# Kernel optimization log

Measured on AMD Instinct MI355X. Metric: run time of the kernel, lower is better.

Reference implementation:

```python
import jax, jax.numpy as jnp
from jax import lax
import numpy as np

WIN = 11
SIGMA = 1.5
VAL_RANGE = 10.0
C1 = (0.01 * VAL_RANGE) ** 2
C2 = (0.03 * VAL_RANGE) ** 2


def _gauss_window():
    # matches pytorch-ssim create_window: normalized 1D gaussian, outer product
    g = np.exp(-((np.arange(WIN) - WIN // 2) ** 2) / (2.0 * SIGMA ** 2))
    g = g / g.sum()
    return jnp.asarray(np.outer(g, g), jnp.float32)


def _blur(x, win):
    # depthwise 11x11 gaussian conv, padding=0 (VALID), per pytorch-ssim with padd=0
    k = x.shape[1]
    kern = jnp.broadcast_to(win[None, None], (k, 1, WIN, WIN)).astype(x.dtype)
    return lax.conv_general_dilated(x, kern, (1, 1), 'VALID', feature_group_count=k)


def setup_inputs() -> dict:
    key = jax.random.key(0)
    ks = jax.random.split(key, 7)
    B, C, H, W = 8, 64, 256, 256
    x = jax.random.normal(ks[0], (B, C, H, W), jnp.float32)
    mask = jax.random.randint(ks[1], (B, H, W), 0, 2, jnp.int32)
    conv_w = jax.random.normal(ks[2], (1, 3, 3, 1), jnp.float32) * 0.3
    w1 = jax.random.normal(ks[3], (C, C), jnp.float32) * (1.0 / np.sqrt(C))
    b1 = jax.random.normal(ks[4], (C,), jnp.float32) * 0.01
    w2 = jax.random.normal(ks[5], (C, C), jnp.float32) * (1.0 / np.sqrt(C))
    b2 = jax.random.normal(ks[6], (C,), jnp.float32) * 0.01
    return {'x': x, 'mask': mask, 'conv_w': conv_w, 'w1': w1, 'b1': b1, 'w2': w2, 'b2': b2}


def reference(x, mask, conv_w, w1, b1, w2, b2):
    B, C, H, W = x.shape
    m = mask.astype(x.dtype)[:, None]  # [B,1,H,W]

    # ChannelPool: max/mean/min over channel dim -> [B,3,H,W]
    xc = jnp.stack([x.max(axis=1), x.mean(axis=1), x.min(axis=1)], axis=1)

    # ChannelNorm: masked per-sample, per-channel mean / unbiased std; zero outside mask
    n = m.sum(axis=(2, 3), keepdims=True)                       # [B,1,1,1]
    mean = (xc * m).sum(axis=(2, 3), keepdims=True) / n
    var = (((xc - mean) ** 2) * m).sum(axis=(2, 3), keepdims=True) / (n - 1.0)
    xf = (xc - mean) / jnp.sqrt(var) * m                        # [B,3,H,W]

    # Pairwise SSIM between xf channels (3) and x channels (C), vectorized
    win = _gauss_window()
    mu_f = _blur(xf, win)                                       # [B,3,H',W']
    mu_x = _blur(x, win)                                        # [B,C,H',W']
    ef2 = _blur(xf * xf, win)
    ex2 = _blur(x * x, win)
    prod = (xf[:, :, None] * x[:, None]).reshape(B, 3 * C, H, W)
    Hp, Wp = H - WIN + 1, W - WIN + 1
    exf = _blur(prod, win).reshape(B, 3, C, Hp, Wp)

    mu1 = mu_f[:, :, None]                                      # [B,3,1,H',W']
    mu2 = mu_x[:, None]                                         # [B,1,C,H',W']
    s1 = ef2[:, :, None] - mu1 ** 2
    s2 = ex2[:, None] - mu2 ** 2
    s12 = exf - mu1 * mu2
    ssim_map = ((2 * mu1 * mu2 + C1) * (2 * s12 + C2)) / ((mu1 ** 2 + mu2 ** 2 + C1) * (s1 + s2 + C2))
    ssim_info = ssim_map.mean(axis=(3, 4))                      # [B,3,C]

    # spatial Conv2d(3,1,(3,1),pad=(1,0)) on [B,3,C,1], then ReLU, MLP, Sigmoid
    h = lax.conv_general_dilated(ssim_info[..., None], conv_w, (1, 1), ((1, 1), (0, 0)))
    h = jax.nn.relu(h).reshape(B, C)
    h = jax.nn.relu(h @ w1.T + b1)
    h = jax.nn.sigmoid(h @ w2.T + b2)
    return h, ssim_info
```

## Files before the change

### kernel.cpp

```cpp
#include <hip/hip_runtime.h>
#include <cmath>

#define Bn   8
#define Cn   64
#define HWc  65536
#define HPc  246
#define HPWPc 60516
#define C1v  0.01f
#define C2v  0.09f

static __device__ __forceinline__ void gauss11(float* gw) {
    double gg[11]; double s = 0.0;
#pragma unroll
    for (int j = 0; j < 11; ++j) { double d = (double)(j - 5); gg[j] = exp(-(d * d) / 4.5); s += gg[j]; }
#pragma unroll
    for (int j = 0; j < 11; ++j) gw[j] = (float)(gg[j] / s);
}

static __device__ __forceinline__ float4 f4z() { return make_float4(0.f, 0.f, 0.f, 0.f); }
static __device__ __forceinline__ float4 f4scale(float g, const float4 v) {
    return make_float4(g * v.x, g * v.y, g * v.z, g * v.w);
}
static __device__ __forceinline__ void f4add(float4& a, const float4 v) {
    a.x += v.x; a.y += v.y; a.z += v.z; a.w += v.w;
}
static __device__ __forceinline__ void f4fma(float4& a, const float4 u, const float4 v) {
    a.x = fmaf(u.x, v.x, a.x); a.y = fmaf(u.y, v.y, a.y);
    a.z = fmaf(u.z, v.z, a.z); a.w = fmaf(u.w, v.w, a.w);
}

static __device__ __forceinline__ void hblur4(const float* vb, int base, const float* gw, float* out4) {
    float w[14];
#pragma unroll
    for (int m = 0; m < 14; ++m) w[m] = vb[base + m];
#pragma unroll
    for (int j = 0; j < 4; ++j) {
        float s = 0.f;
#pragma unroll
        for (int k = 0; k < 11; ++k) s = fmaf(gw[k], w[j + k], s);
        out4[j] = s;
    }
}

__global__ __launch_bounds__(256) void k1_stats(const float* __restrict__ x, const int* __restrict__ mask,
                                                float* __restrict__ xcf, float* __restrict__ stats) {
    const int b = blockIdx.y;
    const int p0 = blockIdx.x * 1024 + threadIdx.x * 4;
    const float4* xp = (const float4*)(x + (size_t)b * Cn * HWc) + (p0 >> 2);
    float4 v = xp[0];
    float4 vmax = v, vmin = v, vsum = v;
#pragma unroll 4
    for (int c = 1; c < Cn; ++c) {
        float4 u = xp[(size_t)c * (HWc / 4)];
        vmax.x = fmaxf(vmax.x, u.x); vmax.y = fmaxf(vmax.y, u.y);
        vmax.z = fmaxf(vmax.z, u.z); vmax.w = fmaxf(vmax.w, u.w);
        vmin.x = fminf(vmin.x, u.x); vmin.y = fminf(vmin.y, u.y);
        vmin.z = fminf(vmin.z, u.z); vmin.w = fminf(vmin.w, u.w);
        vsum.x += u.x; vsum.y += u.y; vsum.z += u.z; vsum.w += u.w;
    }
    float4 vmean = make_float4(vsum.x * (1.f / 64.f), vsum.y * (1.f / 64.f),
                               vsum.z * (1.f / 64.f), vsum.w * (1.f / 64.f));
    *(float4*)(xcf + (size_t)(b * 3 + 0) * HWc + p0) = vmax;
    *(float4*)(xcf + (size_t)(b * 3 + 1) * HWc + p0) = vmean;
    *(float4*)(xcf + (size_t)(b * 3 + 2) * HWc + p0) = vmin;
    int4 mv = *(const int4*)(mask + (size_t)b * HWc + p0);
    float m0 = (float)mv.x, m1 = (float)mv.y, m2 = (float)mv.z, m3 = (float)mv.w;
    float r[7];
    r[0] = m0 + m1 + m2 + m3;
    r[1] = vmax.x * m0 + vmax.y * m1 + vmax.z * m2 + vmax.w * m3;
    r[2] = vmean.x * m0 + vmean.y * m1 + vmean.z * m2 + vmean.w * m3;
    r[3] = vmin.x * m0 + vmin.y * m1 + vmin.z * m2 + vmin.w * m3;
    r[4] = vmax.x * vmax.x * m0 + vmax.y * vmax.y * m1 + vmax.z * vmax.z * m2 + vmax.w * vmax.w * m3;
    r[5] = vmean.x * vmean.x * m0 + vmean.y * vmean.y * m1 + vmean.z * vmean.z * m2 + vmean.w * vmean.w * m3;
    r[6] = vmin.x * vmin.x * m0 + vmin.y * vmin.y * m1 + vmin.z * vmin.z * m2 + vmin.w * vmin.w * m3;
#pragma unroll
    for (int k = 0; k < 7; ++k) {
        float vv = r[k];
#pragma unroll
        for (int off = 32; off > 0; off >>= 1) vv += __shfl_down(vv, off);
        if ((threadIdx.x & 63) == 0) atomicAdd(&stats[b * 8 + k], vv);
    }
}

__global__ __launch_bounds__(256) void k3_xf(float* __restrict__ xcf, const int* __restrict__ mask,
                                             const float* __restrict__ stats) {
    const int b = blockIdx.z, i = blockIdx.y;
    const int p0 = blockIdx.x * 1024 + threadIdx.x * 4;
    const float* st = stats + b * 8;
    const float n = st[0];
    const float s1 = st[1 + i], s2 = st[4 + i];
    const float mean = s1 / n;
    const float var = (s2 - s1 * s1 / n) / (n - 1.0f);
    const float rstd = rsqrtf(var);
    float4* p = (float4*)(xcf + (size_t)(b * 3 + i) * HWc + p0);
    float4 v = *p;
    int4 mv = *(const int4*)(mask + (size_t)b * HWc + p0);
    v.x = (v.x - mean) * rstd * (float)mv.x;
    v.y = (v.y - mean) * rstd * (float)mv.y;
    v.z = (v.z - mean) * rstd * (float)mv.z;
    v.w = (v.w - mean) * rstd * (float)mv.w;
    *p = v;
}

__global__ __launch_bounds__(256) void k4_blur3(const float* __restrict__ xf, float* __restrict__ muf,
                                                float* __restrict__ ef2g) {
    __shared__ __align__(16) float fin[42 * 44];
    __shared__ __align__(16) float vba[32 * 52];
    __shared__ __align__(16) float vbb[32 * 52];
    const int t = threadIdx.x;
    const int bi = blockIdx.z;
    const int y0 = blockIdx.y * 32, x0 = blockIdx.x * 32;
    float gw[11]; gauss11(gw);
    const float* src = xf + (size_t)bi * HWc;
    for (int q = t; q < 42 * 11; q += 256) {
        int row = q / 11, cg = q % 11;
        int gr = min(y0 + row, 255), gc = min(x0 + cg * 4, 252);
        *(float4*)&fin[row * 44 + cg * 4] = *(const float4*)(src + gr * 256 + gc);
    }
    __syncthreads();
    if (t < 88) {
        int rg = t / 11, cg = t % 11, colo = cg * 4;
        float4 aa[4], ab[4];
#pragma unroll
        for (int r = 0; r < 4; ++r) { aa[r] = f4z(); ab[r] = f4z(); }
#pragma unroll
        for (int k = 0; k < 14; ++k) {
            float4 v = *(const float4*)&fin[(4 * rg + k) * 44 + colo];
#pragma unroll
            for (int r = 0; r < 4; ++r) {
                int kk = k - r;
                if (kk >= 0 && kk <= 10) {
                    float4 tv = f4scale(gw[kk], v);
                    f4add(aa[r], tv);
                    f4fma(ab[r], tv, v);
                }
            }
        }
#pragma unroll
        for (int r = 0; r < 4; ++r) {
            int so = (4 * rg + r) * 52 + colo;
            *(float4*)&vba[so] = aa[r];
            *(float4*)&vbb[so] = ab[r];
        }
    }
    __syncthreads();
    {
        int erow = t >> 3, ecg = t & 7;
        int oyy = y0 + erow;
        int base = erow * 52 + ecg * 4;
        float o1[4], o2[4];
        hblur4(vba, base, gw, o1);
        hblur4(vbb, base, gw, o2);
        if (oyy < HPc) {
            size_t ob = (size_t)bi * HPWPc + (size_t)oyy * HPc;
#pragma unroll
            for (int j = 0; j < 4; ++j) {
                int ox = x0 + ecg * 4 + j;
                if (ox < HPc) { muf[ob + ox] = o1[j]; ef2g[ob + ox] = o2[j]; }
            }
        }
    }
}

__global__ __launch_bounds__(256, 2) void k5_main(const float* __restrict__ x, const float* __restrict__ xf,
                                                  const float* __restrict__ muf, const float* __restrict__ ef2g,
                                                  float* __restrict__ ssum) {
    __shared__ __align__(16) float xin[42 * 44];
    __shared__ __align__(16) float f0in[42 * 44];
    __shared__ __align__(16) float f1in[42 * 44];
    __shared__ __align__(16) float f2in[42 * 44];
    __shared__ __align__(16) float vbx[32 * 52];
    __shared__ __align__(16) float vbq[32 * 52];
    __shared__ __align__(16) float vb0[32 * 52];
    __shared__ __align__(16) float vb1a[32 * 52];
    __shared__ __align__(16) float vb2a[32 * 52];
    const int t = threadIdx.x;
    const int b = blockIdx.z;
    const int y0 = blockIdx.y * 32, x0 = blockIdx.x * 32;
    float gw[11]; gauss11(gw);
    {
        const float* f0p = xf + (size_t)(b * 3 + 0) * HWc;
        const float* f1p = xf + (size_t)(b * 3 + 1) * HWc;
        const float* f2p = xf + (size_t)(b * 3 + 2) * HWc;
        for (int q = t; q < 42 * 11; q += 256) {
            int row = q / 11, cg = q % 11;
            int gr = min(y0 + row, 255), gc = min(x0 + cg * 4, 252);
            int go = gr * 256 + gc;
            int lo = row * 44 + cg * 4;
            *(float4*)&f0in[lo] = *(const float4*)(f0p + go);
            *(float4*)&f1in[lo] = *(const float4*)(f1p + go);
            *(float4*)&f2in[lo] = *(const float4*)(f2p + go);
        }
    }
    const int erow = t >> 3;
    const int ecg = t & 7;
    const int oy = y0 + erow;
    float Am[3][4], A2C1[3][4], S1C2[3][4], validf[4];
#pragma unroll
    for (int j = 0; j < 4; ++j) {
        int ox = x0 + ecg * 4 + j;
        bool vld = (oy < HPc) && (ox < HPc);
        validf[j] = vld ? 1.0f : 0.0f;
#pragma unroll
        for (int i = 0; i < 3; ++i) {
            float mu1 = 0.f, e2 = 0.f;
            if (vld) {
                size_t o = (size_t)(b * 3 + i) * HPWPc + (size_t)oy * HPc + ox;
                mu1 = muf[o]; e2 = ef2g[o];
            }
            Am[i][j] = mu1;
            A2C1[i][j] = fmaf(mu1, mu1, C1v);
            S1C2[i][j] = (e2 - mu1 * mu1) + C2v;
        }
    }
    const float* xb = x + (size_t)b * Cn * HWc;
    for (int c = 0; c < Cn; ++c) {
        {
            const float* xp = xb + (size_t)c * HWc;
            for (int q = t; q < 42 * 11; q += 256) {
                int row = q / 11, cg = q % 11;
                int gr = min(y0 + row, 255), gc = min(x0 + cg * 4, 252);
                *(float4*)&xin[row * 44 + cg * 4] = *(const float4*)(xp + gr * 256 + gc);
            }
        }
        __syncthreads();
        if (t < 88) {
            int rg = t / 11;
            int cg = t % 11;
            int colo = cg * 4;
            float4 ax[4], aq[4], a0[4], a1[4], a2[4];
#pragma unroll
            for (int r = 0; r < 4; ++r) { ax[r] = f4z(); aq[r] = f4z(); a0[r] = f4z(); a1[r] = f4z(); a2[r] = f4z(); }
#pragma unroll
            for (int k = 0; k < 14; ++k) {
                int ro = (4 * rg + k) * 44 + colo;
                float4 xv = *(const float4*)&xin[ro];
                float4 f0 = *(const float4*)&f0in[ro];
                float4 f1 = *(const float4*)&f1in[ro];
                float4 f2 = *(const float4*)&f2in[ro];
#pragma unroll
                for (int r = 0; r < 4; ++r) {
                    int kk = k - r;
                    if (kk >= 0 && kk <= 10) {
                        float4 tv = f4scale(gw[kk], xv);
                        f4add(ax[r], tv);
                        f4fma(aq[r], tv, xv);
                        f4fma(a0[r], tv, f0);
                        f4fma(a1[r], tv, f1);
                        f4fma(a2[r], tv, f2);
                    }
                }
            }
#pragma unroll
            for (int r = 0; r < 4; ++r) {
                int so = (4 * rg + r) * 52 + colo;
                *(float4*)&vbx[so] = ax[r];
                *(float4*)&vbq[so] = aq[r];
                *(float4*)&vb0[so] = a0[r];
                *(float4*)&vb1a[so] = a1[r];
                *(float4*)&vb2a[so] = a2[r];
            }
        }
        __syncthreads();
        {
            const int base = erow * 52 + ecg * 4;
            float mu2[4], bx2[4], bp0[4], bp1[4], bp2[4];
            hblur4(vbx, base, gw, mu2);
            hblur4(vbq, base, gw, bx2);
            hblur4(vb0, base, gw, bp0);
            hblur4(vb1a, base, gw, bp1);
            hblur4(vb2a, base, gw, bp2);
            float sa0 = 0.f, sa1 = 0.f, sa2 = 0.f;
#pragma unroll
            for (int j = 0; j < 4; ++j) {
                float m2 = mu2[j];
                float m2sq = m2 * m2;
                float s2 = bx2[j] - m2sq;
                {
                    float am = Am[0][j] * m2;
                    float num = fmaf(2.f, am, C1v) * fmaf(2.f, bp0[j] - am, C2v);
                    float den = (A2C1[0][j] + m2sq) * (S1C2[0][j] + s2);
                    sa0 += validf[j] * num * __builtin_amdgcn_rcpf(den);
                }
                {
                    float am = Am[1][j] * m2;
                    float num = fmaf(2.f, am, C1v) * fmaf(2.f, bp1[j] - am, C2v);
                    float den = (A2C1[1][j] + m2sq) * (S1C2[1][j] + s2);
                    sa1 += validf[j] * num * __builtin_amdgcn_rcpf(den);
                }
                {
                    float am = Am[2][j] * m2;
                    float num = fmaf(2.f, am, C1v) * fmaf(2.f, bp2[j] - am, C2v);
                    float den = (A2C1[2][j] + m2sq) * (S1C2[2][j] + s2);
                    sa2 += validf[j] * num * __builtin_amdgcn_rcpf(den);
                }
            }
#pragma unroll
            for (int off = 32; off > 0; off >>= 1) {
                sa0 += __shfl_down(sa0, off);
                sa1 += __shfl_down(sa1, off);
                sa2 += __shfl_down(sa2, off);
            }
            if ((t & 63) == 0) {
                atomicAdd(&ssum[(b * 3 + 0) * 64 + c], sa0);
                atomicAdd(&ssum[(b * 3 + 1) * 64 + c], sa1);
                atomicAdd(&ssum[(b * 3 + 2) * 64 + c], sa2);
            }
        }
    }
}

__global__ __launch_bounds__(512) void k6_head(const float* __restrict__ ssum, const float* __restrict__ cw,
                                               const float* __restrict__ w1, const float* __restrict__ b1,
                                               const float* __restrict__ w2, const float* __restrict__ b2,
                                               float* __restrict__ out) {
    __shared__ float si[1536];
    __shared__ float h0[512];
    __shared__ float h1[512];
    const int t = threadIdx.x;
    const float inv = 1.0f / (float)HPWPc;
    for (int idx = t; idx < 1536; idx += 512) {
        float v = ssum[idx] * inv;
        si[idx] = v;
        out[512 + idx] = v;
    }
    __syncthreads();
    const int b = t >> 6, y = t & 63;
    float acc = 0.f;
#pragma unroll
    for (int i = 0; i < 3; ++i) {
#pragma unroll
        for (int kh = 0; kh < 3; ++kh) {
            int yy = y + kh - 1;
            if (yy >= 0 && yy < 64) acc = fmaf(si[(b * 3 + i) * 64 + yy], cw[i * 3 + kh], acc);
        }
    }
    h0[t] = fmaxf(acc, 0.f);
    __syncthreads();
    float a1 = b1[y];
    for (int c = 0; c < 64; ++c) a1 = fmaf(h0[(b << 6) + c], w1[(y << 6) + c], a1);
    h1[t] = fmaxf(a1, 0.f);
    __syncthreads();
    float a2 = b2[y];
    for (int c = 0; c < 64; ++c) a2 = fmaf(h1[(b << 6) + c], w2[(y << 6) + c], a2);
    out[t] = 1.f / (1.f + expf(-a2));
}

extern "C" void kernel_launch(void* const* d_in, const int* in_sizes, int n_in,
                              void* d_out, int out_size, void* d_ws, size_t ws_size,
                              hipStream_t stream) {
    const float* x      = (const float*)d_in[0];
    const int*   mask   = (const int*)d_in[1];
    const float* conv_w = (const float*)d_in[2];
    const float* w1     = (const float*)d_in[3];
    const float* b1     = (const float*)d_in[4];
    const float* w2     = (const float*)d_in[5];
    const float* b2     = (const float*)d_in[6];
    float* out = (float*)d_out;

    float* wsf   = (float*)d_ws;
    float* stats = wsf;
    float* ssum  = wsf + 64;
    float* xcf   = wsf + 1600;
    float* muf   = xcf + (size_t)Bn * 3 * HWc;
    float* ef2   = muf + (size_t)Bn * 3 * HPWPc;

    hipMemsetAsync(d_ws, 0, 6400, stream);

    k1_stats<<<dim3(64, 8), 256, 0, stream>>>(x, mask, xcf, stats);
    k3_xf<<<dim3(64, 3, 8), 256, 0, stream>>>(xcf, mask, stats);
    k4_blur3<<<dim3(8, 8, 24), 256, 0, stream>>>(xcf, muf, ef2);
    k5_main<<<dim3(8, 8, 8), 256, 0, stream>>>(x, xcf, muf, ef2, ssum);
    k6_head<<<1, 512, 0, stream>>>(ssum, conv_w, w1, b1, w2, b2, out);
}
```

Measured before the change: 706.3 us.

## Fuse normalization into blur kernels, read x directly, interleave blur buffers, DPP reductions

Removes the separate normalization kernel and instead applies the masked mean/rstd normalization on the fly inside the blur and main SSIM kernels. The main kernel now reads x rows straight from global memory for the vertical pass, with 176 threads each handling 2 output rows instead of 88 handling 4. It stores the five vertical-blur results interleaved in one shared buffer so the horizontal pass can use float4 loads. It also replaces shfl-based wave reductions with DPP row operations and raises the occupancy hint to 3 blocks per SM, at the cost of redundant global reads across overlapping row windows and an extra barrier per channel.

```diff
diff --git a/kernel.cpp b/kernel.cpp
--- a/kernel.cpp
+++ b/kernel.cpp
@@ -29,17 +29,14 @@
     a.z = fmaf(u.z, v.z, a.z); a.w = fmaf(u.w, v.w, a.w);
 }
 
-static __device__ __forceinline__ void hblur4(const float* vb, int base, const float* gw, float* out4) {
-    float w[14];
-#pragma unroll
-    for (int m = 0; m < 14; ++m) w[m] = vb[base + m];
-#pragma unroll
-    for (int j = 0; j < 4; ++j) {
-        float s = 0.f;
-#pragma unroll
-        for (int k = 0; k < 11; ++k) s = fmaf(gw[k], w[j + k], s);
-        out4[j] = s;
-    }
+static __device__ __forceinline__ float wave_sum64(float v) {
+    v += __int_as_float(__builtin_amdgcn_update_dpp(0, __float_as_int(v), 0x111, 0xf, 0xf, true));
+    v += __int_as_float(__builtin_amdgcn_update_dpp(0, __float_as_int(v), 0x112, 0xf, 0xf, true));
+    v += __int_as_float(__builtin_amdgcn_update_dpp(0, __float_as_int(v), 0x114, 0xf, 0xf, true));
+    v += __int_as_float(__builtin_amdgcn_update_dpp(0, __float_as_int(v), 0x118, 0xf, 0xf, true));
+    v += __int_as_float(__builtin_amdgcn_update_dpp(0, __float_as_int(v), 0x142, 0xf, 0xf, true));
+    v += __int_as_float(__builtin_amdgcn_update_dpp(0, __float_as_int(v), 0x143, 0xf, 0xf, true));
+    return v;
 }
 
 __global__ __launch_bounds__(256) void k1_stats(const float* __restrict__ x, const int* __restrict__ mask,
@@ -75,125 +72,125 @@
     r[6] = vmin.x * vmin.x * m0 + vmin.y * vmin.y * m1 + vmin.z * vmin.z * m2 + vmin.w * vmin.w * m3;
 #pragma unroll
     for (int k = 0; k < 7; ++k) {
-        float vv = r[k];
-#pragma unroll
-        for (int off = 32; off > 0; off >>= 1) vv += __shfl_down(vv, off);
-        if ((threadIdx.x & 63) == 0) atomicAdd(&stats[b * 8 + k], vv);
-    }
-}
-
-__global__ __launch_bounds__(256) void k3_xf(float* __restrict__ xcf, const int* __restrict__ mask,
-                                             const float* __restrict__ stats) {
-    const int b = blockIdx.z, i = blockIdx.y;
-    const int p0 = blockIdx.x * 1024 + threadIdx.x * 4;
-    const float* st = stats + b * 8;
-    const float n = st[0];
-    const float s1 = st[1 + i], s2 = st[4 + i];
-    const float mean = s1 / n;
-    const float var = (s2 - s1 * s1 / n) / (n - 1.0f);
-    const float rstd = rsqrtf(var);
-    float4* p = (float4*)(xcf + (size_t)(b * 3 + i) * HWc + p0);
-    float4 v = *p;
-    int4 mv = *(const int4*)(mask + (size_t)b * HWc + p0);
-    v.x = (v.x - mean) * rstd * (float)mv.x;
-    v.y = (v.y - mean) * rstd * (float)mv.y;
-    v.z = (v.z - mean) * rstd * (float)mv.z;
-    v.w = (v.w - mean) * rstd * (float)mv.w;
-    *p = v;
-}
-
-__global__ __launch_bounds__(256) void k4_blur3(const float* __restrict__ xf, float* __restrict__ muf,
-                                                float* __restrict__ ef2g) {
-    __shared__ __align__(16) float fin[42 * 44];
-    __shared__ __align__(16) float vba[32 * 52];
-    __shared__ __align__(16) float vbb[32 * 52];
+        float vv = wave_sum64(r[k]);
+        if ((threadIdx.x & 63) == 63) atomicAdd(&stats[b * 8 + k], vv);
+    }
+}
+
+__global__ __launch_bounds__(256) void k4_blur3(const float* __restrict__ xc, const int* __restrict__ mask,
+                                                const float* __restrict__ stats,
+                                                float* __restrict__ muf, float* __restrict__ ef2g) {
+    __shared__ __align__(16) float vb2[32 * 92];
     const int t = threadIdx.x;
-    const int bi = blockIdx.z;
+    const int bi = blockIdx.z, b = bi / 3, i = bi % 3;
     const int y0 = blockIdx.y * 32, x0 = blockIdx.x * 32;
     float gw[11]; gauss11(gw);
-    const float* src = xf + (size_t)bi * HWc;
-    for (int q = t; q < 42 * 11; q += 256) {
-        int row = q / 11, cg = q % 11;
-        int gr = min(y0 + row, 255), gc = min(x0 + cg * 4, 252);
-        *(float4*)&fin[row * 44 + cg * 4] = *(const float4*)(src + gr * 256 + gc);
-    }
-    __syncthreads();
-    if (t < 88) {
-        int rg = t / 11, cg = t % 11, colo = cg * 4;
-        float4 aa[4], ab[4];
-#pragma unroll
-        for (int r = 0; r < 4; ++r) { aa[r] = f4z(); ab[r] = f4z(); }
-#pragma unroll
-        for (int k = 0; k < 14; ++k) {
-            float4 v = *(const float4*)&fin[(4 * rg + k) * 44 + colo];
-#pragma unroll
-            for (int r = 0; r < 4; ++r) {
-                int kk = k - r;
+    const float nst = stats[b * 8 + 0];
+    const float s1 = stats[b * 8 + 1 + i], s2 = stats[b * 8 + 4 + i];
+    const float mean = s1 / nst;
+    const float rstd = rsqrtf((s2 - s1 * s1 / nst) / (nst - 1.0f));
+    if (t < 176) {
+        const int rg = t / 11, cg = t % 11, colo = cg * 4;
+        const int gcb = min(x0 + colo, 252);
+        const float* xp = xc + (size_t)bi * HWc;
+        const int* mp = mask + (size_t)b * HWc;
+        float4 av[2], ab[2];
+#pragma unroll
+        for (int r = 0; r < 2; ++r) { av[r] = f4z(); ab[r] = f4z(); }
+#pragma unroll
+        for (int k = 0; k < 12; ++k) {
+            int gr = min(y0 + 2 * rg + k, 255);
+            float4 v = *(const float4*)(xp + gr * 256 + gcb);
+            int4 mv = *(const int4*)(mp + gr * 256 + gcb);
+            float4 f;
+            f.x = (v.x - mean) * rstd * (float)mv.x;
+            f.y = (v.y - mean) * rstd * (float)mv.y;
+            f.z = (v.z - mean) * rstd * (float)mv.z;
+            f.w = (v.w - mean) * rstd * (float)mv.w;
+            if (k <= 10) { float4 tv = f4scale(gw[k], f); f4add(av[0], tv); f4fma(ab[0], tv, f); }
+            if (k >= 1)  { float4 tv = f4scale(gw[k - 1], f); f4add(av[1], tv); f4fma(ab[1], tv, f); }
+        }
+#pragma unroll
+        for (int r = 0; r < 2; ++r) {
+            float* dst = &vb2[(2 * rg + r) * 92 + colo * 2];
+            *(float4*)&dst[0] = make_float4(av[r].x, ab[r].x, av[r].y, ab[r].y);
+            *(float4*)&dst[4] = make_float4(av[r].z, ab[r].z, av[r].w, ab[r].w);
+        }
+    }
+    __syncthreads();
+    {
+        const int erow = t >> 3, ecg = t & 7;
+        const int oy = y0 + erow;
+        const float* src = &vb2[erow * 92 + ecg * 8];
+        float fl[28];
+#pragma unroll
+        for (int q = 0; q < 7; ++q) *(float4*)&fl[q * 4] = *(const float4*)(src + q * 4);
+        float acc[2][4];
+#pragma unroll
+        for (int f = 0; f < 2; ++f)
+#pragma unroll
+            for (int j = 0; j < 4; ++j) acc[f][j] = 0.f;
+#pragma unroll
+        for (int m = 0; m < 14; ++m) {
+#pragma unroll
+            for (int j = 0; j < 4; ++j) {
+                int kk = m - j;
                 if (kk >= 0 && kk <= 10) {
-                    float4 tv = f4scale(gw[kk], v);
-                    f4add(aa[r], tv);
-                    f4fma(ab[r], tv, v);
-                }
-            }
-        }
-#pragma unroll
-        for (int r = 0; r < 4; ++r) {
-            int so = (4 * rg + r) * 52 + colo;
-            *(float4*)&vba[so] = aa[r];
-            *(float4*)&vbb[so] = ab[r];
-        }
-    }
-    __syncthreads();
-    {
-        int erow = t >> 3, ecg = t & 7;
-        int oyy = y0 + erow;
-        int base = erow * 52 + ecg * 4;
-        float o1[4], o2[4];
-        hblur4(vba, base, gw, o1);
-        hblur4(vbb, base, gw, o2);
-        if (oyy < HPc) {
-            size_t ob = (size_t)bi * HPWPc + (size_t)oyy * HPc;
+                    acc[0][j] = fmaf(gw[kk], fl[m * 2 + 0], acc[0][j]);
+                    acc[1][j] = fmaf(gw[kk], fl[m * 2 + 1], acc[1][j]);
+                }
+            }
+        }
+        if (oy < HPc) {
+            size_t ob = (size_t)bi * HPWPc + (size_t)oy * HPc;
 #pragma unroll
             for (int j = 0; j < 4; ++j) {
                 int ox = x0 + ecg * 4 + j;
-                if (ox < HPc) { muf[ob + ox] = o1[j]; ef2g[ob + ox] = o2[j]; }
-            }
-        }
-    }
-}
-
-__global__ __launch_bounds__(256, 2) void k5_main(const float* __restrict__ x, const float* __restrict__ xf,
+                if (ox < HPc) { muf[ob + ox] = acc[0][j]; ef2g[ob + ox] = acc[1][j]; }
+            }
+        }
+    }
+}
+
+__global__ __launch_bounds__(256, 3) void k5_main(const float* __restrict__ x, const float* __restrict__ xc,
+                                                  const int* __restrict__ mask, const float* __restrict__ stats,
                                                   const float* __restrict__ muf, const float* __restrict__ ef2g,
                                                   float* __restrict__ ssum) {
-    __shared__ __align__(16) float xin[42 * 44];
     __shared__ __align__(16) float f0in[42 * 44];
     __shared__ __align__(16) float f1in[42 * 44];
     __shared__ __align__(16) float f2in[42 * 44];
-    __shared__ __align__(16) float vbx[32 * 52];
-    __shared__ __align__(16) float vbq[32 * 52];
-    __shared__ __align__(16) float vb0[32 * 52];
-    __shared__ __align__(16) float vb1a[32 * 52];
-    __shared__ __align__(16) float vb2a[32 * 52];
+    __shared__ __align__(16) float vb5[32 * 228];
     const int t = threadIdx.x;
     const int b = blockIdx.z;
     const int y0 = blockIdx.y * 32, x0 = blockIdx.x * 32;
     float gw[11]; gauss11(gw);
-    {
-        const float* f0p = xf + (size_t)(b * 3 + 0) * HWc;
-        const float* f1p = xf + (size_t)(b * 3 + 1) * HWc;
-        const float* f2p = xf + (size_t)(b * 3 + 2) * HWc;
-        for (int q = t; q < 42 * 11; q += 256) {
-            int row = q / 11, cg = q % 11;
-            int gr = min(y0 + row, 255), gc = min(x0 + cg * 4, 252);
-            int go = gr * 256 + gc;
-            int lo = row * 44 + cg * 4;
-            *(float4*)&f0in[lo] = *(const float4*)(f0p + go);
-            *(float4*)&f1in[lo] = *(const float4*)(f1p + go);
-            *(float4*)&f2in[lo] = *(const float4*)(f2p + go);
-        }
-    }
-    const int erow = t >> 3;
-    const int ecg = t & 7;
+    const float nst = stats[b * 8 + 0];
+    float mean[3], rstd[3];
+#pragma unroll
+    for (int i = 0; i < 3; ++i) {
+        float s1 = stats[b * 8 + 1 + i], s2 = stats[b * 8 + 4 + i];
+        mean[i] = s1 / nst;
+        rstd[i] = rsqrtf((s2 - s1 * s1 / nst) / (nst - 1.0f));
+    }
+    for (int q = t; q < 42 * 11; q += 256) {
+        int row = q / 11, cg = q % 11;
+        int gr = min(y0 + row, 255), gc = min(x0 + cg * 4, 252);
+        int go = gr * 256 + gc;
+        int lo = row * 44 + cg * 4;
+        int4 mv = *(const int4*)(mask + (size_t)b * HWc + go);
+        float m0 = (float)mv.x, m1 = (float)mv.y, m2 = (float)mv.z, m3 = (float)mv.w;
+#pragma unroll
+        for (int i = 0; i < 3; ++i) {
+            float4 v = *(const float4*)(xc + (size_t)(b * 3 + i) * HWc + go);
+            v.x = (v.x - mean[i]) * rstd[i] * m0;
+            v.y = (v.y - mean[i]) * rstd[i] * m1;
+            v.z = (v.z - mean[i]) * rstd[i] * m2;
+            v.w = (v.w - mean[i]) * rstd[i] * m3;
+            float* dst = (i == 0) ? f0in : (i == 1) ? f1in : f2in;
+            *(float4*)&dst[lo] = v;
+        }
+    }
+    const int erow = t >> 3, ecg = t & 7;
     const int oy = y0 + erow;
     float Am[3][4], A2C1[3][4], S1C2[3][4], validf[4];
 #pragma unroll
@@ -213,100 +210,106 @@
             S1C2[i][j] = (e2 - mu1 * mu1) + C2v;
         }
     }
+    __syncthreads();
     const float* xb = x + (size_t)b * Cn * HWc;
+    const int vrg = t / 11, vcg = t % 11, vcolo = vcg * 4;
+    const int gcb = min(x0 + vcolo, 252);
+    const bool vact = (t < 176);
     for (int c = 0; c < Cn; ++c) {
-        {
+        if (vact) {
             const float* xp = xb + (size_t)c * HWc;
-            for (int q = t; q < 42 * 11; q += 256) {
-                int row = q / 11, cg = q % 11;
-                int gr = min(y0 + row, 255), gc = min(x0 + cg * 4, 252);
-                *(float4*)&xin[row * 44 + cg * 4] = *(const float4*)(xp + gr * 256 + gc);
-            }
-        }
-        __syncthreads();
-        if (t < 88) {
-            int rg = t / 11;
-            int cg = t % 11;
-            int colo = cg * 4;
-            float4 ax[4], aq[4], a0[4], a1[4], a2[4];
-#pragma unroll
-            for (int r = 0; r < 4; ++r) { ax[r] = f4z(); aq[r] = f4z(); a0[r] = f4z(); a1[r] = f4z(); a2[r] = f4z(); }
-#pragma unroll
-            for (int k = 0; k < 14; ++k) {
-                int ro = (4 * rg + k) * 44 + colo;
-                float4 xv = *(const float4*)&xin[ro];
+            float4 a[2][5];
+#pragma unroll
+            for (int r = 0; r < 2; ++r)
+#pragma unroll
+                for (int f = 0; f < 5; ++f) a[r][f] = f4z();
+#pragma unroll
+            for (int k = 0; k < 12; ++k) {
+                int gr = min(y0 + 2 * vrg + k, 255);
+                float4 xv = *(const float4*)(xp + gr * 256 + gcb);
+                int ro = (2 * vrg + k) * 44 + vcolo;
                 float4 f0 = *(const float4*)&f0in[ro];
                 float4 f1 = *(const float4*)&f1in[ro];
                 float4 f2 = *(const float4*)&f2in[ro];
-#pragma unroll
-                for (int r = 0; r < 4; ++r) {
-                    int kk = k - r;
-                    if (kk >= 0 && kk <= 10) {
-                        float4 tv = f4scale(gw[kk], xv);
-                        f4add(ax[r], tv);
-                        f4fma(aq[r], tv, xv);
-                        f4fma(a0[r], tv, f0);
-                        f4fma(a1[r], tv, f1);
-                        f4fma(a2[r], tv, f2);
-                    }
-                }
-            }
-#pragma unroll
-            for (int r = 0; r < 4; ++r) {
-                int so = (4 * rg + r) * 52 + colo;
-                *(float4*)&vbx[so] = ax[r];
-                *(float4*)&vbq[so] = aq[r];
-                *(float4*)&vb0[so] = a0[r];
-                *(float4*)&vb1a[so] = a1[r];
-                *(float4*)&vb2a[so] = a2[r];
+                if (k <= 10) {
+                    float4 tv = f4scale(gw[k], xv);
+                    f4add(a[0][0], tv); f4fma(a[0][1], tv, xv);
+                    f4fma(a[0][2], tv, f0); f4fma(a[0][3], tv, f1); f4fma(a[0][4], tv, f2);
+                }
+                if (k >= 1) {
+                    float4 tv = f4scale(gw[k - 1], xv);
+                    f4add(a[1][0], tv); f4fma(a[1][1], tv, xv);
+                    f4fma(a[1][2], tv, f0); f4fma(a[1][3], tv, f1); f4fma(a[1][4], tv, f2);
+                }
+            }
+#pragma unroll
+            for (int r = 0; r < 2; ++r) {
+                float4 A = a[r][0], Bq = a[r][1], P0 = a[r][2], P1 = a[r][3], P2 = a[r][4];
+                float* dst = &vb5[(2 * vrg + r) * 228 + vcolo * 5];
+                *(float4*)&dst[0]  = make_float4(A.x, Bq.x, P0.x, P1.x);
+                *(float4*)&dst[4]  = make_float4(P2.x, A.y, Bq.y, P0.y);
+                *(float4*)&dst[8]  = make_float4(P1.y, P2.y, A.z, Bq.z);
+                *(float4*)&dst[12] = make_float4(P0.z, P1.z, P2.z, A.w);
+                *(float4*)&dst[16] = make_float4(Bq.w, P0.w, P1.w, P2.w);
             }
         }
         __syncthreads();
         {
-            const int base = erow * 52 + ecg * 4;
-            float mu2[4], bx2[4], bp0[4], bp1[4], bp2[4];
-            hblur4(vbx, base, gw, mu2);
-            hblur4(vbq, base, gw, bx2);
-            hblur4(vb0, base, gw, bp0);
-            hblur4(vb1a, base, gw, bp1);
-            hblur4(vb2a, base, gw, bp2);
+            const float* src = &vb5[erow * 228 + ecg * 20];
+            float fl[72];
+#pragma unroll
+            for (int q = 0; q < 18; ++q) *(float4*)&fl[q * 4] = *(const float4*)(src + q * 4);
+            float hacc[5][4];
+#pragma unroll
+            for (int f = 0; f < 5; ++f)
+#pragma unroll
+                for (int j = 0; j < 4; ++j) hacc[f][j] = 0.f;
+#pragma unroll
+            for (int m = 0; m < 14; ++m) {
+#pragma unroll
+                for (int j = 0; j < 4; ++j) {
+                    int kk = m - j;
+                    if (kk >= 0 && kk <= 10) {
+#pragma unroll
+                        for (int f = 0; f < 5; ++f) hacc[f][j] = fmaf(gw[kk], fl[m * 5 + f], hacc[f][j]);
+                    }
+                }
+            }
             float sa0 = 0.f, sa1 = 0.f, sa2 = 0.f;
 #pragma unroll
             for (int j = 0; j < 4; ++j) {
-                float m2 = mu2[j];
+                float m2 = hacc[0][j];
                 float m2sq = m2 * m2;
-                float s2 = bx2[j] - m2sq;
+                float s2 = hacc[1][j] - m2sq;
                 {
                     float am = Am[0][j] * m2;
-                    float num = fmaf(2.f, am, C1v) * fmaf(2.f, bp0[j] - am, C2v);
+                    float num = fmaf(2.f, am, C1v) * fmaf(2.f, hacc[2][j] - am, C2v);
                     float den = (A2C1[0][j] + m2sq) * (S1C2[0][j] + s2);
                     sa0 += validf[j] * num * __builtin_amdgcn_rcpf(den);
                 }
                 {
                     float am = Am[1][j] * m2;
-                    float num = fmaf(2.f, am, C1v) * fmaf(2.f, bp1[j] - am, C2v);
+                    float num = fmaf(2.f, am, C1v) * fmaf(2.f, hacc[3][j] - am, C2v);
                     float den = (A2C1[1][j] + m2sq) * (S1C2[1][j] + s2);
                     sa1 += validf[j] * num * __builtin_amdgcn_rcpf(den);
                 }
                 {
                     float am = Am[2][j] * m2;
-                    float num = fmaf(2.f, am, C1v) * fmaf(2.f, bp2[j] - am, C2v);
+                    float num = fmaf(2.f, am, C1v) * fmaf(2.f, hacc[4][j] - am, C2v);
                     float den = (A2C1[2][j] + m2sq) * (S1C2[2][j] + s2);
                     sa2 += validf[j] * num * __builtin_amdgcn_rcpf(den);
                 }
             }
-#pragma unroll
-            for (int off = 32; off > 0; off >>= 1) {
-                sa0 += __shfl_down(sa0, off);
-                sa1 += __shfl_down(sa1, off);
-                sa2 += __shfl_down(sa2, off);
-            }
-            if ((t & 63) == 0) {
+            sa0 = wave_sum64(sa0);
+            sa1 = wave_sum64(sa1);
+            sa2 = wave_sum64(sa2);
+            if ((t & 63) == 63) {
                 atomicAdd(&ssum[(b * 3 + 0) * 64 + c], sa0);
                 atomicAdd(&ssum[(b * 3 + 1) * 64 + c], sa1);
                 atomicAdd(&ssum[(b * 3 + 2) * 64 + c], sa2);
             }
         }
+        __syncthreads();
     }
 }
 
@@ -368,8 +371,7 @@
     hipMemsetAsync(d_ws, 0, 6400, stream);
 
     k1_stats<<<dim3(64, 8), 256, 0, stream>>>(x, mask, xcf, stats);
-    k3_xf<<<dim3(64, 3, 8), 256, 0, stream>>>(xcf, mask, stats);
-    k4_blur3<<<dim3(8, 8, 24), 256, 0, stream>>>(xcf, muf, ef2);
-    k5_main<<<dim3(8, 8, 8), 256, 0, stream>>>(x, xcf, muf, ef2, ssum);
+    k4_blur3<<<dim3(8, 8, 24), 256, 0, stream>>>(xcf, mask, stats, muf, ef2);
+    k5_main<<<dim3(8, 8, 8), 256, 0, stream>>>(x, xcf, mask, stats, muf, ef2, ssum);
     k6_head<<<1, 512, 0, stream>>>(ssum, conv_w, w1, b1, w2, b2, out);
 }
```

Result: slower. 1.981 ms (+180.4%).
